# Kernel optimization log

Hardware: AMD Instinct MI355X
Metric: run time of the kernel (lower is better)

## Reference

```python
import jax, jax.numpy as jnp
import numpy as np

B, N_OBJ, N_REL = 32, 16, 64
C, H, W = 1024, 50, 50
POOL, SR = 7, 2          # roi_pool_size, sampling_ratio
SPATIAL_SCALE = 1.0      # boxes are pre-scaled to fmap coords by scale_bboxes
DIMS = [1024, 1024, 512] # lin_obj_dim
IMG = 800                # square frame -> the original's h/w swap bug is a no-op


def setup_inputs() -> dict:
    key = jax.random.key(0)
    ks = jax.random.split(key, 8)
    fmap = jax.random.normal(ks[0], (B, C, H, W), dtype=jnp.float32)
    # valid boxes in image coords: x1<x2, y1<y2, inside [0, IMG]
    xy1 = jax.random.uniform(ks[1], (B, N_OBJ, 2), minval=0.0, maxval=600.0)
    wh = jax.random.uniform(ks[2], (B, N_OBJ, 2), minval=50.0, maxval=200.0)
    bboxes = jnp.concatenate([xy1, xy1 + wh], axis=-1).astype(jnp.float32)
    num_obj = jnp.full((B,), N_OBJ, dtype=jnp.int32)
    num_rels = jnp.full((B,), N_REL, dtype=jnp.int32)
    obj_pairs = jax.random.randint(ks[3], (B, N_REL, 2), 0, N_OBJ, dtype=jnp.int32)
    s1 = 1.0 / np.sqrt(DIMS[0]).astype(np.float32)
    s2 = 1.0 / np.sqrt(DIMS[1]).astype(np.float32)
    W1 = jax.random.uniform(ks[4], (DIMS[0], DIMS[1]), minval=-s1, maxval=s1, dtype=jnp.float32)
    b1 = jax.random.uniform(ks[5], (DIMS[1],), minval=-s1, maxval=s1, dtype=jnp.float32)
    W2 = jax.random.uniform(ks[6], (DIMS[1], DIMS[2]), minval=-s2, maxval=s2, dtype=jnp.float32)
    b2 = jax.random.uniform(ks[7], (DIMS[2],), minval=-s2, maxval=s2, dtype=jnp.float32)
    return dict(frame_feature_map=fmap, bboxes=bboxes, num_obj=num_obj,
                obj_pairs=obj_pairs, num_rels=num_rels,
                frame_width=IMG, frame_height=IMG,
                W1=W1, b1=b1, W2=W2, b2=b2)


def _interp_axis(coord, size):
    # torchvision RoIAlign (aligned=False) bilinear precompute along one axis
    valid = ((coord >= -1.0) & (coord <= size)).astype(coord.dtype)
    c = jnp.maximum(coord, 0.0)
    low = jnp.floor(c).astype(jnp.int32)
    at_edge = low >= size - 1
    low = jnp.minimum(low, size - 1)
    high = jnp.minimum(low + 1, size - 1)
    l = jnp.where(at_edge, 0.0, c - low.astype(coord.dtype))
    return low, high, 1.0 - l, l, valid


def roi_align(fmap, boxes, batch_idx, pool, sr, scale):
    # fmap [B,C,H,W]; boxes [R,4] (x1,y1,x2,y2); returns [R,pool,pool,C]
    _, Cc, Hc, Wc = fmap.shape
    x1, y1, x2, y2 = (boxes[:, i] * scale for i in range(4))
    roi_w = jnp.maximum(x2 - x1, 1.0)
    roi_h = jnp.maximum(y2 - y1, 1.0)
    # sample offsets (separable): bin ph, subsample iy -> ph + (iy+0.5)/sr, in bin units
    grid = (jnp.arange(pool, dtype=fmap.dtype)[:, None]
            + (jnp.arange(sr, dtype=fmap.dtype)[None, :] + 0.5) / sr).reshape(-1)  # [pool*sr]
    ys = y1[:, None] + (roi_h / pool)[:, None] * grid[None, :]  # [R, Sy]
    xs = x1[:, None] + (roi_w / pool)[:, None] * grid[None, :]  # [R, Sx]
    yl, yh, wy0, wy1, vy = _interp_axis(ys, Hc)
    xl, xh, wx0, wx1, vx = _interp_axis(xs, Wc)
    b = batch_idx[:, None, None]

    def g(yi, xi):
        # advanced indices split by ':' -> result [R, Sy, Sx, C]
        return fmap[b, :, yi[:, :, None], xi[:, None, :]]

    val = (wy0[:, :, None, None] * (wx0[:, None, :, None] * g(yl, xl)
                                    + wx1[:, None, :, None] * g(yl, xh))
           + wy1[:, :, None, None] * (wx0[:, None, :, None] * g(yh, xl)
                                      + wx1[:, None, :, None] * g(yh, xh)))
    val = val * (vy[:, :, None, None] * vx[:, None, :, None])  # out-of-range points -> 0
    R = boxes.shape[0]
    # average the sr x sr samples per bin (count = sr*sr, as in torchvision)
    return val.reshape(R, pool, sr, pool, sr, Cc).mean(axis=(2, 4))


def reference(frame_feature_map, bboxes, num_obj, obj_pairs, num_rels,
              frame_width, frame_height, W1, b1, W2, b2):
    Bn, Nmax = bboxes.shape[:2]
    # scale_bboxes -- faithful to the original (note its im_height/im_width swap)
    im_height, im_width = frame_width, frame_height
    fh, fw = frame_feature_map.shape[-2:]
    hs = fh / (im_height * 1.0)
    ws = fw / (im_width * 1.0)
    scaled = bboxes * jnp.asarray([ws, hs, ws, hs], dtype=bboxes.dtype)
    boxes = scaled.reshape(-1, 4)                              # full counts: concat == flatten
    batch_idx = jnp.repeat(jnp.arange(Bn, dtype=jnp.int32), Nmax)
    roi = roi_align(frame_feature_map, boxes, batch_idx, POOL, SR, SPATIAL_SCALE)  # [R,7,7,C]
    # lin_obj_net: Linear+ReLU stack applied on the channel (last) dim
    h = jax.nn.relu(roi @ W1 + b1)
    h = jax.nn.relu(h @ W2 + b2)                               # [R,7,7,512]
    feat = h.mean(axis=(1, 2))                                 # AvgPool2d(7x7) -> flatten: [R,512]
    # pair_features: gather two object vectors per relation and average
    obj_off = jnp.concatenate([jnp.zeros((1,), jnp.int32),
                               jnp.cumsum(num_obj)[:-1].astype(jnp.int32)])
    idx = obj_off[:, None, None] + obj_pairs                   # [B, N_REL, 2]
    f0 = feat[idx[..., 0].reshape(-1)]
    f1 = feat[idx[..., 1].reshape(-1)]
    return 0.5 * (f0 + f1)                                     # [sum(num_rels), 512]
```

## Files before the change

kernel.cpp:

```cpp
#include <hip/hip_runtime.h>

#define DEV __device__ __forceinline__

typedef unsigned short u16;
typedef short bf16x8 __attribute__((ext_vector_type(8)));
typedef float f32x4 __attribute__((ext_vector_type(4)));

#define BB    32
#define NOBJ  16
#define NREL  64
#define CCH   1024
#define FHW   50
#define HW    2500
#define NROI  512
#define MROWS 25088
#define D1    1024
#define D2    512

DEV u16 f2bf(float f) {
  unsigned u = __float_as_uint(f);
  unsigned r = (u + 0x7FFFu + ((u >> 16) & 1u)) >> 16;
  return (u16)r;
}
DEV float bf2f(u16 h) { return __uint_as_float((unsigned)h << 16); }
DEV unsigned pk(float lo, float hi) { return (unsigned)f2bf(lo) | ((unsigned)f2bf(hi) << 16); }

using gvoid = __attribute__((address_space(1))) const void;
using svoid = __attribute__((address_space(3))) void;
DEV void gl_lds16(const void* g, void* s) {
  __builtin_amdgcn_global_load_lds((gvoid*)g, (svoid*)s, 16, 0, 0);
}

__global__ __launch_bounds__(256) void k_transpose_cast(
    const float* __restrict__ in, u16* __restrict__ out, int R, int C) {
  __shared__ float tile[64][65];
  const int b = blockIdx.z;
  const int c0 = blockIdx.x * 64;
  const int r0 = blockIdx.y * 64;
  const float* inb = in + (size_t)b * R * C;
  u16* outb = out + (size_t)b * R * C;
  const int t = threadIdx.x;
  {
    const int rr = t >> 4;
    const int cq = (t & 15) * 4;
#pragma unroll
    for (int it = 0; it < 4; ++it) {
      int rl = rr + it * 16;
      int r = r0 + rl;
      int c = c0 + cq;
      if (c + 3 < C) {
        float4 v = *reinterpret_cast<const float4*>(&inb[(size_t)r * C + c]);
        tile[rl][cq + 0] = v.x; tile[rl][cq + 1] = v.y;
        tile[rl][cq + 2] = v.z; tile[rl][cq + 3] = v.w;
      } else {
#pragma unroll
        for (int j = 0; j < 4; ++j)
          tile[rl][cq + j] = (c + j < C) ? inb[(size_t)r * C + c + j] : 0.f;
      }
    }
  }
  __syncthreads();
  {
    const int c = t >> 2;
    const int rch = (t & 3) * 8;
    if (c0 + c < C) {
#pragma unroll
      for (int half = 0; half < 2; ++half) {
        int rb = rch + half * 32;
        uint4 o;
        o.x = pk(tile[rb + 0][c], tile[rb + 1][c]);
        o.y = pk(tile[rb + 2][c], tile[rb + 3][c]);
        o.z = pk(tile[rb + 4][c], tile[rb + 5][c]);
        o.w = pk(tile[rb + 6][c], tile[rb + 7][c]);
        *reinterpret_cast<uint4*>(&outb[(size_t)(c0 + c) * R + r0 + rb]) = o;
      }
    }
  }
}

DEV void acc8v(uint4 v, float w, float* a) {
  a[0] = fmaf(w, bf2f((u16)(v.x & 0xffffu)), a[0]);
  a[1] = fmaf(w, bf2f((u16)(v.x >> 16)), a[1]);
  a[2] = fmaf(w, bf2f((u16)(v.y & 0xffffu)), a[2]);
  a[3] = fmaf(w, bf2f((u16)(v.y >> 16)), a[3]);
  a[4] = fmaf(w, bf2f((u16)(v.z & 0xffffu)), a[4]);
  a[5] = fmaf(w, bf2f((u16)(v.z >> 16)), a[5]);
  a[6] = fmaf(w, bf2f((u16)(v.w & 0xffffu)), a[6]);
  a[7] = fmaf(w, bf2f((u16)(v.w >> 16)), a[7]);
}

template <int YC, int XC>
DEV void bin_accum(const u16* bt, const int* yrow, const float* yw,
                   const int* xidx, const float* xw, float* a) {
  uint4 v[YC * XC];
#pragma unroll
  for (int jy = 0; jy < YC; ++jy)
#pragma unroll
    for (int jx = 0; jx < XC; ++jx)
      v[jy * XC + jx] =
          *reinterpret_cast<const uint4*>(bt + (size_t)(yrow[jy] + xidx[jx]) * CCH);
#pragma unroll
  for (int jy = 0; jy < YC; ++jy)
#pragma unroll
    for (int jx = 0; jx < XC; ++jx)
      acc8v(v[jy * XC + jx], yw[jy] * xw[jx], a);
}

__global__ __launch_bounds__(128) void k_roi_fast(
    const u16* __restrict__ fmT, const float* __restrict__ bboxes,
    const int* __restrict__ pfw, const int* __restrict__ pfh,
    u16* __restrict__ Aout) {
  const int r = blockIdx.x;
  const int py = blockIdx.y;
  const int b = r >> 4;
  const int t = threadIdx.x;
  const int c0 = t * 8;

  __shared__ int s_cnt[2][7];
  __shared__ int s_idx[2][7][4];
  __shared__ float s_wgt[2][7][4];

  int axis = -1, p = 0;
  if (t < 7) { axis = 0; p = t; }
  else if (t >= 64 && t < 71) { axis = 1; p = t - 64; }
  if (axis >= 0) {
    float fwf = (float)pfw[0], fhf = (float)pfh[0];
    float hs = (float)FHW / fwf;
    float wsc = (float)FHW / fhf;
    float v1 = bboxes[r * 4 + (axis == 0 ? 1 : 0)] * (axis == 0 ? hs : wsc);
    float v2 = bboxes[r * 4 + (axis == 0 ? 3 : 2)] * (axis == 0 ? hs : wsc);
    float ext = fmaxf(v2 - v1, 1.0f);
    int idx[4]; float wgt[4]; int cnt = 0;
#pragma unroll
    for (int j = 0; j < 2; ++j) {
      float g = (float)p + (j ? 0.75f : 0.25f);
      float coord = v1 + (ext / 7.0f) * g;
      float valid = (coord >= -1.0f && coord <= 50.0f) ? 1.0f : 0.0f;
      float cc = fmaxf(coord, 0.0f);
      int lo = (int)floorf(cc);
      bool edge = (lo >= FHW - 1);
      lo = min(lo, FHW - 1);
      int hi = min(lo + 1, FHW - 1);
      float l = edge ? 0.0f : (cc - (float)lo);
      float pr_i[2]; int pr_x[2];
      pr_x[0] = lo; pr_i[0] = valid * (1.0f - l);
      pr_x[1] = hi; pr_i[1] = valid * l;
#pragma unroll
      for (int e = 0; e < 2; ++e) {
        if (pr_i[e] != 0.0f) {
          bool found = false;
          for (int q = 0; q < cnt; ++q)
            if (idx[q] == pr_x[e]) { wgt[q] += pr_i[e]; found = true; }
          if (!found) { idx[cnt] = pr_x[e]; wgt[cnt] = pr_i[e]; ++cnt; }
        }
      }
    }
    s_cnt[axis][p] = cnt;
#pragma unroll
    for (int q = 0; q < 4; ++q) {
      s_idx[axis][p][q] = (q < cnt) ? idx[q] : 0;
      s_wgt[axis][p][q] = (q < cnt) ? wgt[q] : 0.0f;
    }
  }
  __syncthreads();

  const u16* bt = fmT + (size_t)b * HW * CCH + c0;

  const int ycnt = s_cnt[0][py];
  int yrow[3]; float yw[3];
#pragma unroll
  for (int q = 0; q < 3; ++q) {
    yrow[q] = s_idx[0][py][q] * FHW;
    yw[q] = s_wgt[0][py][q];
  }

  for (int px = 0; px < 7; ++px) {
    const int xcnt = s_cnt[1][px];
    int xidx[3]; float xw[3];
#pragma unroll
    for (int q = 0; q < 3; ++q) {
      xidx[q] = s_idx[1][px][q];
      xw[q] = s_wgt[1][px][q];
    }
    float a[8] = {};
    switch (ycnt * 4 + xcnt) {
      case 1 * 4 + 1: bin_accum<1, 1>(bt, yrow, yw, xidx, xw, a); break;
      case 1 * 4 + 2: bin_accum<1, 2>(bt, yrow, yw, xidx, xw, a); break;
      case 1 * 4 + 3: bin_accum<1, 3>(bt, yrow, yw, xidx, xw, a); break;
      case 2 * 4 + 1: bin_accum<2, 1>(bt, yrow, yw, xidx, xw, a); break;
      case 2 * 4 + 2: bin_accum<2, 2>(bt, yrow, yw, xidx, xw, a); break;
      case 2 * 4 + 3: bin_accum<2, 3>(bt, yrow, yw, xidx, xw, a); break;
      case 3 * 4 + 1: bin_accum<3, 1>(bt, yrow, yw, xidx, xw, a); break;
      case 3 * 4 + 2: bin_accum<3, 2>(bt, yrow, yw, xidx, xw, a); break;
      case 3 * 4 + 3: bin_accum<3, 3>(bt, yrow, yw, xidx, xw, a); break;
      default: break;
    }
    u16* dst = Aout + (size_t)(r * 49 + py * 7 + px) * CCH + c0;
    uint4 o;
    o.x = pk(a[0] * 0.25f, a[1] * 0.25f);
    o.y = pk(a[2] * 0.25f, a[3] * 0.25f);
    o.z = pk(a[4] * 0.25f, a[5] * 0.25f);
    o.w = pk(a[6] * 0.25f, a[7] * 0.25f);
    *reinterpret_cast<uint4*>(dst) = o;
  }
}

template <int K, int N, int OBF>
__global__ __launch_bounds__(256) void k_gemm(
    const u16* __restrict__ A, const u16* __restrict__ Bt,
    const float* __restrict__ bias, void* __restrict__ Out) {
  __shared__ alignas(16) u16 As[128 * 32];
  __shared__ alignas(16) u16 Bs[128 * 32];
  const int t = threadIdx.x;
  const int lane = t & 63, w = t >> 6;
  const int wr = w >> 1, wc = w & 1;
  const int NT = N / 128;
  const int bid = blockIdx.x;
  const int chunk = (int)(gridDim.x >> 3);
  const int swz = (bid & 7) * chunk + (bid >> 3);
  const size_t m0 = (size_t)(swz / NT) * 128;
  const int n0 = (swz % NT) * 128;
  f32x4 acc[4][4] = {};
  const int srow = t >> 2;
  const int skc = (t & 3) * 8;
  for (int ks = 0; ks < K / 32; ++ks) {
    const int k0 = ks * 32;
    if (ks) __syncthreads();
    gl_lds16(A + (m0 + srow) * K + k0 + skc, &As[(size_t)t * 8]);
    gl_lds16(A + (m0 + 64 + srow) * K + k0 + skc, &As[(size_t)(t + 256) * 8]);
    gl_lds16(Bt + (size_t)(n0 + srow) * K + k0 + skc, &Bs[(size_t)t * 8]);
    gl_lds16(Bt + (size_t)(n0 + 64 + srow) * K + k0 + skc, &Bs[(size_t)(t + 256) * 8]);
    __syncthreads();
    const int koff = (lane >> 4) * 8;
    bf16x8 av[4], bv[4];
#pragma unroll
    for (int m = 0; m < 4; ++m)
      av[m] = *reinterpret_cast<const bf16x8*>(&As[(wr * 64 + m * 16 + (lane & 15)) * 32 + koff]);
#pragma unroll
    for (int n = 0; n < 4; ++n)
      bv[n] = *reinterpret_cast<const bf16x8*>(&Bs[(wc * 64 + n * 16 + (lane & 15)) * 32 + koff]);
#pragma unroll
    for (int m = 0; m < 4; ++m)
#pragma unroll
      for (int n = 0; n < 4; ++n)
        asm("v_mfma_f32_16x16x32_bf16 %0, %1, %2, %0"
            : "+v"(acc[m][n]) : "v"(av[m]), "v"(bv[n]));
  }
  asm volatile("s_nop 7\n\ts_nop 7\n\ts_nop 7" ::);
#pragma unroll
  for (int n = 0; n < 4; ++n) {
    int col = n0 + wc * 64 + n * 16 + (lane & 15);
    float bb = bias[col];
#pragma unroll
    for (int m = 0; m < 4; ++m) {
      size_t row0 = m0 + wr * 64 + m * 16 + (lane >> 4) * 4;
#pragma unroll
      for (int qq = 0; qq < 4; ++qq) {
        float v = fmaxf(acc[m][n][qq] + bb, 0.0f);
        if (OBF) ((u16*)Out)[(row0 + qq) * N + col] = f2bf(v);
        else     ((float*)Out)[(row0 + qq) * N + col] = v;
      }
    }
  }
}

__global__ __launch_bounds__(256) void k_mean(const u16* __restrict__ H2,
                                              float* __restrict__ feat) {
  const int r = blockIdx.x;
  const int c = threadIdx.x * 2;
  float s0 = 0.f, s1 = 0.f;
#pragma unroll
  for (int qq = 0; qq < 49; ++qq) {
    unsigned v = *reinterpret_cast<const unsigned*>(&H2[((size_t)r * 49 + qq) * D2 + c]);
    s0 += bf2f((u16)(v & 0xffffu));
    s1 += bf2f((u16)(v >> 16));
  }
  feat[(size_t)r * D2 + c] = s0 * (1.0f / 49.0f);
  feat[(size_t)r * D2 + c + 1] = s1 * (1.0f / 49.0f);
}

__global__ __launch_bounds__(256) void k_pairs(
    const float* __restrict__ feat, const int* __restrict__ num_obj,
    const int* __restrict__ pairs, float* __restrict__ out) {
  int r = blockIdx.x;
  int b = r >> 6;
  int off = 0;
  for (int i = 0; i < b; ++i) off += num_obj[i];
  int g0 = off + pairs[r * 2 + 0];
  int g1 = off + pairs[r * 2 + 1];
  for (int c = threadIdx.x; c < D2; c += 256) {
    out[(size_t)r * D2 + c] = 0.5f * (feat[(size_t)g0 * D2 + c] + feat[(size_t)g1 * D2 + c]);
  }
}

extern "C" void kernel_launch(void* const* d_in, const int* in_sizes, int n_in,
                              void* d_out, int out_size, void* d_ws, size_t ws_size,
                              hipStream_t stream) {
  const float* fmap = (const float*)d_in[0];
  const float* bboxes = (const float*)d_in[1];
  const int* num_obj = (const int*)d_in[2];
  const int* obj_pairs = (const int*)d_in[3];
  const int* pfw = (const int*)d_in[5];
  const int* pfh = (const int*)d_in[6];
  const float* W1 = (const float*)d_in[7];
  const float* b1 = (const float*)d_in[8];
  const float* W2 = (const float*)d_in[9];
  const float* b2 = (const float*)d_in[10];
  float* out = (float*)d_out;

  const size_t SZ_FMT = (size_t)BB * HW * CCH * 2;
  const size_t SZ_A   = (size_t)MROWS * D1 * 2;
  const size_t SZ_H1  = (size_t)MROWS * D1 * 2;
  const size_t SZ_W1B = (size_t)D1 * D1 * 2;
  const size_t SZ_W2B = (size_t)D1 * D2 * 2;

  char* ws = (char*)d_ws;
  u16 *fmT, *A, *H1, *W1b, *W2b, *H2b;
  float *feat;
  fmT = (u16*)ws;
  A = (u16*)(ws + SZ_FMT);
  H1 = (u16*)(ws + SZ_FMT + SZ_A);
  W1b = (u16*)(ws + SZ_FMT + SZ_A + SZ_H1);
  W2b = (u16*)(ws + SZ_FMT + SZ_A + SZ_H1 + SZ_W1B);
  feat = (float*)(ws + SZ_FMT + SZ_A + SZ_H1 + SZ_W1B + SZ_W2B);
  H2b = fmT;

  k_transpose_cast<<<dim3(16, 16, 1), 256, 0, stream>>>(W1, W1b, D1, D1);
  k_transpose_cast<<<dim3(8, 16, 1), 256, 0, stream>>>(W2, W2b, D1, D2);

  k_transpose_cast<<<dim3(40, 16, BB), 256, 0, stream>>>(fmap, fmT, CCH, HW);
  k_roi_fast<<<dim3(NROI, 7), 128, 0, stream>>>(fmT, bboxes, pfw, pfh, A);

  k_gemm<D1, D1, 1><<<(MROWS / 128) * (D1 / 128), 256, 0, stream>>>(A, W1b, b1, (void*)H1);
  k_gemm<D1, D2, 1><<<(MROWS / 128) * (D2 / 128), 256, 0, stream>>>(H1, W2b, b2, (void*)H2b);
  k_mean<<<NROI, 256, 0, stream>>>(H2b, feat);
  k_pairs<<<BB * NREL, 256, 0, stream>>>(feat, num_obj, obj_pairs, out);
}
```

Before: 269.8 us.

## Fuse 7x7 mean pooling into second GEMM epilogue and merge weight transposes

The second GEMM epilogue now reduces its ReLU outputs per ROI, first into shared memory with atomics and then into a global feature buffer with atomics. This removes the H2 bf16 intermediate write and the separate mean kernel. The two weight transpose launches are merged into one kernel, and a zero-fill kernel is added for the atomic accumulator. The change adds shared and global atomic traffic, and summation order is no longer deterministic.

```diff
diff --git a/kernel.cpp b/kernel.cpp
--- a/kernel.cpp
+++ b/kernel.cpp
@@ -31,15 +31,9 @@
   __builtin_amdgcn_global_load_lds((gvoid*)g, (svoid*)s, 16, 0, 0);
 }
 
-__global__ __launch_bounds__(256) void k_transpose_cast(
-    const float* __restrict__ in, u16* __restrict__ out, int R, int C) {
+DEV void transpose_tile(const float* __restrict__ in, u16* __restrict__ out,
+                        int R, int C, int c0, int r0, int t) {
   __shared__ float tile[64][65];
-  const int b = blockIdx.z;
-  const int c0 = blockIdx.x * 64;
-  const int r0 = blockIdx.y * 64;
-  const float* inb = in + (size_t)b * R * C;
-  u16* outb = out + (size_t)b * R * C;
-  const int t = threadIdx.x;
   {
     const int rr = t >> 4;
     const int cq = (t & 15) * 4;
@@ -49,13 +43,13 @@
       int r = r0 + rl;
       int c = c0 + cq;
       if (c + 3 < C) {
-        float4 v = *reinterpret_cast<const float4*>(&inb[(size_t)r * C + c]);
+        float4 v = *reinterpret_cast<const float4*>(&in[(size_t)r * C + c]);
         tile[rl][cq + 0] = v.x; tile[rl][cq + 1] = v.y;
         tile[rl][cq + 2] = v.z; tile[rl][cq + 3] = v.w;
       } else {
 #pragma unroll
         for (int j = 0; j < 4; ++j)
-          tile[rl][cq + j] = (c + j < C) ? inb[(size_t)r * C + c + j] : 0.f;
+          tile[rl][cq + j] = (c + j < C) ? in[(size_t)r * C + c + j] : 0.f;
       }
     }
   }
@@ -72,9 +66,28 @@
         o.y = pk(tile[rb + 2][c], tile[rb + 3][c]);
         o.z = pk(tile[rb + 4][c], tile[rb + 5][c]);
         o.w = pk(tile[rb + 6][c], tile[rb + 7][c]);
-        *reinterpret_cast<uint4*>(&outb[(size_t)(c0 + c) * R + r0 + rb]) = o;
+        *reinterpret_cast<uint4*>(&out[(size_t)(c0 + c) * R + r0 + rb]) = o;
       }
     }
+  }
+}
+
+__global__ __launch_bounds__(256) void k_transpose_cast(
+    const float* __restrict__ in, u16* __restrict__ out, int R, int C) {
+  const int b = blockIdx.z;
+  transpose_tile(in + (size_t)b * R * C, out + (size_t)b * R * C, R, C,
+                 blockIdx.x * 64, blockIdx.y * 64, threadIdx.x);
+}
+
+__global__ __launch_bounds__(256) void k_transpose_w12(
+    const float* __restrict__ W1, u16* __restrict__ W1b,
+    const float* __restrict__ W2, u16* __restrict__ W2b) {
+  const int bid = blockIdx.x;
+  if (bid < 256) {
+    transpose_tile(W1, W1b, D1, D1, (bid & 15) * 64, (bid >> 4) * 64, threadIdx.x);
+  } else {
+    const int b2 = bid - 256;
+    transpose_tile(W2, W2b, D1, D2, (b2 & 7) * 64, (b2 >> 3) * 64, threadIdx.x);
   }
 }
 
@@ -205,10 +218,10 @@
   }
 }
 
-template <int K, int N, int OBF>
+template <int K, int N>
 __global__ __launch_bounds__(256) void k_gemm(
     const u16* __restrict__ A, const u16* __restrict__ Bt,
-    const float* __restrict__ bias, void* __restrict__ Out) {
+    const float* __restrict__ bias, u16* __restrict__ Out) {
   __shared__ alignas(16) u16 As[128 * 32];
   __shared__ alignas(16) u16 Bs[128 * 32];
   const int t = threadIdx.x;
@@ -257,26 +270,99 @@
 #pragma unroll
       for (int qq = 0; qq < 4; ++qq) {
         float v = fmaxf(acc[m][n][qq] + bb, 0.0f);
-        if (OBF) ((u16*)Out)[(row0 + qq) * N + col] = f2bf(v);
-        else     ((float*)Out)[(row0 + qq) * N + col] = v;
+        Out[(row0 + qq) * N + col] = f2bf(v);
       }
     }
   }
 }
 
-__global__ __launch_bounds__(256) void k_mean(const u16* __restrict__ H2,
-                                              float* __restrict__ feat) {
-  const int r = blockIdx.x;
-  const int c = threadIdx.x * 2;
-  float s0 = 0.f, s1 = 0.f;
-#pragma unroll
-  for (int qq = 0; qq < 49; ++qq) {
-    unsigned v = *reinterpret_cast<const unsigned*>(&H2[((size_t)r * 49 + qq) * D2 + c]);
-    s0 += bf2f((u16)(v & 0xffffu));
-    s1 += bf2f((u16)(v >> 16));
-  }
-  feat[(size_t)r * D2 + c] = s0 * (1.0f / 49.0f);
-  feat[(size_t)r * D2 + c + 1] = s1 * (1.0f / 49.0f);
+__global__ __launch_bounds__(256) void k_gemm2_fused(
+    const u16* __restrict__ A, const u16* __restrict__ Bt,
+    const float* __restrict__ bias, float* __restrict__ feat) {
+  constexpr int K = D1, N = D2;
+  __shared__ alignas(16) u16 As[128 * 32];
+  __shared__ alignas(16) u16 Bs[128 * 32];
+  __shared__ float sfeat[4][128];
+  const int t = threadIdx.x;
+  const int lane = t & 63, w = t >> 6;
+  const int wr = w >> 1, wc = w & 1;
+  const int NT = N / 128;
+  const int bid = blockIdx.x;
+  const int chunk = (int)(gridDim.x >> 3);
+  const int swz = (bid & 7) * chunk + (bid >> 3);
+  const size_t m0 = (size_t)(swz / NT) * 128;
+  const int n0 = (swz % NT) * 128;
+  f32x4 acc[4][4] = {};
+  const int srow = t >> 2;
+  const int skc = (t & 3) * 8;
+  for (int ks = 0; ks < K / 32; ++ks) {
+    const int k0 = ks * 32;
+    if (ks) __syncthreads();
+    gl_lds16(A + (m0 + srow) * K + k0 + skc, &As[(size_t)t * 8]);
+    gl_lds16(A + (m0 + 64 + srow) * K + k0 + skc, &As[(size_t)(t + 256) * 8]);
+    gl_lds16(Bt + (size_t)(n0 + srow) * K + k0 + skc, &Bs[(size_t)t * 8]);
+    gl_lds16(Bt + (size_t)(n0 + 64 + srow) * K + k0 + skc, &Bs[(size_t)(t + 256) * 8]);
+    __syncthreads();
+    const int koff = (lane >> 4) * 8;
+    bf16x8 av[4], bv[4];
+#pragma unroll
+    for (int m = 0; m < 4; ++m)
+      av[m] = *reinterpret_cast<const bf16x8*>(&As[(wr * 64 + m * 16 + (lane & 15)) * 32 + koff]);
+#pragma unroll
+    for (int n = 0; n < 4; ++n)
+      bv[n] = *reinterpret_cast<const bf16x8*>(&Bs[(wc * 64 + n * 16 + (lane & 15)) * 32 + koff]);
+#pragma unroll
+    for (int m = 0; m < 4; ++m)
+#pragma unroll
+      for (int n = 0; n < 4; ++n)
+        asm("v_mfma_f32_16x16x32_bf16 %0, %1, %2, %0"
+            : "+v"(acc[m][n]) : "v"(av[m]), "v"(bv[n]));
+  }
+  asm volatile("s_nop 7\n\ts_nop 7\n\ts_nop 7" ::);
+
+  __syncthreads();
+  for (int idx = t; idx < 512; idx += 256) ((float*)sfeat)[idx] = 0.0f;
+  __syncthreads();
+
+  const int roi_base = (int)(m0 / 49);
+#pragma unroll
+  for (int n = 0; n < 4; ++n) {
+    const int col = n0 + wc * 64 + n * 16 + (lane & 15);
+    const int coll = wc * 64 + n * 16 + (lane & 15);
+    const float bb = bias[col];
+#pragma unroll
+    for (int m = 0; m < 4; ++m) {
+      const int row0 = (int)m0 + wr * 64 + m * 16 + (lane >> 4) * 4;
+      float run = 0.0f;
+      int rl_prev = (row0) / 49 - roi_base;
+#pragma unroll
+      for (int qq = 0; qq < 4; ++qq) {
+        const int rl = (row0 + qq) / 49 - roi_base;
+        const float v = fmaxf(acc[m][n][qq] + bb, 0.0f);
+        if (rl != rl_prev) {
+          atomicAdd(&sfeat[rl_prev][coll], run);
+          run = 0.0f;
+          rl_prev = rl;
+        }
+        run += v;
+      }
+      atomicAdd(&sfeat[rl_prev][coll], run);
+    }
+  }
+  __syncthreads();
+
+  for (int idx = t; idx < 512; idx += 256) {
+    const int rl = idx >> 7, cl = idx & 127;
+    const int roi = roi_base + rl;
+    if (roi < NROI) {
+      const float s = sfeat[rl][cl];
+      if (s != 0.0f) atomicAdd(&feat[(size_t)roi * D2 + n0 + cl], s * (1.0f / 49.0f));
+    }
+  }
+}
+
+__global__ __launch_bounds__(256) void k_zero(float4* __restrict__ p) {
+  p[blockIdx.x * 256 + threadIdx.x] = float4{0.f, 0.f, 0.f, 0.f};
 }
 
 __global__ __launch_bounds__(256) void k_pairs(
@@ -315,24 +401,21 @@
   const size_t SZ_W2B = (size_t)D1 * D2 * 2;
 
   char* ws = (char*)d_ws;
-  u16 *fmT, *A, *H1, *W1b, *W2b, *H2b;
-  float *feat;
-  fmT = (u16*)ws;
-  A = (u16*)(ws + SZ_FMT);
-  H1 = (u16*)(ws + SZ_FMT + SZ_A);
-  W1b = (u16*)(ws + SZ_FMT + SZ_A + SZ_H1);
-  W2b = (u16*)(ws + SZ_FMT + SZ_A + SZ_H1 + SZ_W1B);
-  feat = (float*)(ws + SZ_FMT + SZ_A + SZ_H1 + SZ_W1B + SZ_W2B);
-  H2b = fmT;
-
-  k_transpose_cast<<<dim3(16, 16, 1), 256, 0, stream>>>(W1, W1b, D1, D1);
-  k_transpose_cast<<<dim3(8, 16, 1), 256, 0, stream>>>(W2, W2b, D1, D2);
+  u16* fmT = (u16*)ws;
+  u16* A   = (u16*)(ws + SZ_FMT);
+  u16* H1  = (u16*)(ws + SZ_FMT + SZ_A);
+  u16* W1b = (u16*)(ws + SZ_FMT + SZ_A + SZ_H1);
+  u16* W2b = (u16*)(ws + SZ_FMT + SZ_A + SZ_H1 + SZ_W1B);
+  float* feat = (float*)(ws + SZ_FMT + SZ_A + SZ_H1 + SZ_W1B + SZ_W2B);
+
+  k_zero<<<NROI * D2 / 1024, 256, 0, stream>>>((float4*)feat);
+
+  k_transpose_w12<<<384, 256, 0, stream>>>(W1, W1b, W2, W2b);
 
   k_transpose_cast<<<dim3(40, 16, BB), 256, 0, stream>>>(fmap, fmT, CCH, HW);
   k_roi_fast<<<dim3(NROI, 7), 128, 0, stream>>>(fmT, bboxes, pfw, pfh, A);
 
-  k_gemm<D1, D1, 1><<<(MROWS / 128) * (D1 / 128), 256, 0, stream>>>(A, W1b, b1, (void*)H1);
-  k_gemm<D1, D2, 1><<<(MROWS / 128) * (D2 / 128), 256, 0, stream>>>(H1, W2b, b2, (void*)H2b);
-  k_mean<<<NROI, 256, 0, stream>>>(H2b, feat);
+  k_gemm<D1, D1><<<(MROWS / 128) * (D1 / 128), 256, 0, stream>>>(A, W1b, b1, H1);
+  k_gemm2_fused<<<(MROWS / 128) * (D2 / 128), 256, 0, stream>>>(H1, W2b, b2, feat);
   k_pairs<<<BB * NREL, 256, 0, stream>>>(feat, num_obj, obj_pairs, out);
 }
```

Measured after the change: 281.0 us. +4.2%, slower.
